# Optimization experiments

Hardware: AMD Instinct MI355X
Metric: run time of the kernel (lower is better)

## Reference

```python
import jax, jax.numpy as jnp
import numpy as np

NUM_TOURS = 200   # fixed segment count (original: tour_index.max()+1)
EPS = 1e-5        # torch InstanceNorm1d default eps


def setup_inputs() -> dict:
    key = jax.random.key(0)
    ks = jax.random.split(key, 9)
    B, P, D = 64, 2000, 128
    embeddings = jax.random.normal(ks[0], (B, P + 1, D), jnp.float32)
    tour_index = jax.random.randint(ks[1], (B, P), 0, NUM_TOURS, dtype=jnp.int32)
    # tour_combiner: Linear(2D -> D); feedforward: Linear(D -> D); stored as (in, out)
    W1 = jax.random.normal(ks[2], (2 * D, D), jnp.float32) / np.sqrt(2 * D)
    b1 = jax.random.normal(ks[3], (D,), jnp.float32) * 0.01
    W2 = jax.random.normal(ks[4], (D, D), jnp.float32) / np.sqrt(D)
    b2 = jax.random.normal(ks[5], (D,), jnp.float32) * 0.01
    # InstanceNorm1d affine params (per channel)
    gamma = 1.0 + 0.1 * jax.random.normal(ks[6], (D,), jnp.float32)
    beta = 0.1 * jax.random.normal(ks[7], (D,), jnp.float32)
    return {
        "batch_size": B, "num_customers": P,
        "tour_index": tour_index, "embeddings": embeddings,
        "W1": W1, "b1": b1, "W2": W2, "b2": b2,
        "gamma": gamma, "beta": beta,
    }


def reference(batch_size, num_customers, tour_index, embeddings, W1, b1, W2, b2, gamma, beta):
    B, P = batch_size, num_customers
    D = embeddings.shape[-1]
    cust = embeddings[:, 1:]                                  # (B, P, D)
    # tour-level segment sum (scatter_add over tour ids, per batch)
    flat_idx = (tour_index + jnp.arange(B, dtype=tour_index.dtype)[:, None] * NUM_TOURS).reshape(-1)
    tour_emb = jax.ops.segment_sum(cust.reshape(B * P, D), flat_idx,
                                   num_segments=B * NUM_TOURS).reshape(B, NUM_TOURS, D)
    # gather tour embedding back to each customer
    cust_tour = jnp.take_along_axis(tour_emb, tour_index[:, :, None], axis=1)  # (B, P, D)
    # concat -> linear -> relu -> linear
    combined = jnp.concatenate([cust, cust_tour], axis=-1)    # (B, P, 2D)
    h = jax.nn.relu(combined @ W1 + b1)
    h = h @ W2 + b2
    # residual + instance norm over the customer axis, per channel
    added = cust + h
    mean = jnp.mean(added, axis=1, keepdims=True)
    var = jnp.var(added, axis=1, keepdims=True)
    normed = (added - mean) * jax.lax.rsqrt(var + EPS) * gamma + beta
    return jnp.concatenate([embeddings[:, :1], normed], axis=1)
```

## Files before the change

kernel.cpp:

```cpp
#include <hip/hip_runtime.h>
#include <stdint.h>

typedef unsigned short u16;
typedef __attribute__((ext_vector_type(8))) short short8;
typedef __attribute__((ext_vector_type(4))) float floatx4;

constexpr int B_ = 64, P_ = 2000, D_ = 128, T_ = 200;

__device__ __forceinline__ u16 f2bf(float f) {
  union { float f; uint32_t u; } v; v.f = f;
  return (u16)((v.u + 0x7fffu + ((v.u >> 16) & 1u)) >> 16);
}

__global__ __launch_bounds__(256) void k_pre(
    const int* __restrict__ tidx, int* __restrict__ list,
    int* __restrict__ goff, int* __restrict__ gcnt,
    const float* __restrict__ W1, const float* __restrict__ W2,
    u16* __restrict__ w1f, u16* __restrict__ w2f, float* __restrict__ ssum) {
  __shared__ int tix[P_];
  __shared__ int cnt[256], scan[256], cur[256];
  const int bid = blockIdx.x, tid = threadIdx.x;

  if (bid >= 64) {
    if (bid < 128) {
      ssum[(bid - 64) * 256 + tid] = 0.f;
      return;
    }
    int t = (bid - 128) * 256 + tid;
    if (t >= 6144) return;
    const float* W = (t < 4096) ? W1 : W2;
    u16* dst = (t < 4096) ? w1f : w2f;
    int fid = (t < 4096) ? t : t - 4096;
    int lane = fid & 63;
    int nt = (fid >> 6) & 7;
    int ks = fid >> 9;
    int quad = lane >> 4, c = lane & 15;
    int k0 = ks * 32 + quad * 8;
#pragma unroll
    for (int j = 0; j < 8; ++j)
      dst[(size_t)fid * 8 + j] = f2bf(W[(k0 + j) * D_ + nt * 16 + c]);
    return;
  }

  const int b = bid;
  cnt[tid] = 0;
  for (int i = tid; i < P_; i += 256) tix[i] = tidx[b * P_ + i];
  __syncthreads();
  for (int i = tid; i < P_; i += 256) atomicAdd(&cnt[tix[i]], 1);
  __syncthreads();
  scan[tid] = cnt[tid];
  __syncthreads();
  for (int s = 1; s < 256; s <<= 1) {
    int v = (tid >= s) ? scan[tid - s] : 0;
    __syncthreads();
    scan[tid] += v;
    __syncthreads();
  }
  int excl = scan[tid] - cnt[tid];
  if (tid < T_) {
    goff[b * T_ + tid] = excl;
    gcnt[b * T_ + tid] = cnt[tid];
  }
  cur[tid] = excl;
  __syncthreads();
  for (int i = tid; i < P_; i += 256) {
    int slot = atomicAdd(&cur[tix[i]], 1);
    list[b * P_ + slot] = i;
  }
}

__global__ __launch_bounds__(256) void k_gather(const float* __restrict__ emb,
                                                const int* __restrict__ list,
                                                const int* __restrict__ goff,
                                                const int* __restrict__ gcnt,
                                                u16* __restrict__ tourb) {
  const int tid = threadIdx.x;
  const int lane = tid & 63, wv = tid >> 6;
  const int seg = blockIdx.x * 4 + wv;
  const int b = seg / T_;
  const int off = goff[seg], cn = gcnt[seg];
  const int* lstb = list + b * P_;
  const float* eb = emb + ((size_t)(b * 2001 + 1)) * D_ + lane * 2;
  float sx = 0.f, sy = 0.f;
  for (int i = 0; i < cn; i += 8) {
    int pr[8];
#pragma unroll
    for (int j = 0; j < 8; ++j)
      if (i + j < cn) pr[j] = lstb[off + i + j];
    float2 v[8];
#pragma unroll
    for (int j = 0; j < 8; ++j)
      if (i + j < cn) v[j] = *(const float2*)(eb + (size_t)pr[j] * D_);
#pragma unroll
    for (int j = 0; j < 8; ++j)
      if (i + j < cn) { sx += v[j].x; sy += v[j].y; }
  }
  uint32_t pk = (uint32_t)f2bf(sx) | ((uint32_t)f2bf(sy) << 16);
  ((uint32_t*)(tourb + (size_t)seg * D_))[lane] = pk;
}

__global__ __launch_bounds__(256, 8) void k_mlp(
    const int* __restrict__ tidx, const float* __restrict__ emb,
    const u16* __restrict__ tourb,
    const u16* __restrict__ w1f, const u16* __restrict__ w2f,
    const float* __restrict__ b1, const float* __restrict__ b2,
    float* __restrict__ ssum, float* __restrict__ ssq,
    float* __restrict__ out) {
  __shared__ u16 hbuf[64 * 136];
  __shared__ float red[2][2][128];
  const int tid = threadIdx.x;
  const int w = tid >> 6, lane = tid & 63, quad = lane >> 4, c = lane & 15;
  const int base = blockIdx.x * 64;
  const int r0 = w * 16;

  for (int i = tid; i < 512; i += 256) ((float*)red)[i] = 0.f;

  const int blo = base / P_;
  const int bhi = (base + 63) / P_;
  const bool straddle = (blo != bhi);
  const int bsplit = bhi * P_;

  const int m0 = base + r0 + c;
  const int ab = m0 / P_, ap = m0 - ab * P_;
  const float* arow = emb + ((size_t)(ab * 2001 + 1 + ap)) * D_;
  const u16* trow = tourb + ((size_t)(ab * T_ + tidx[m0])) * D_;

  float bias1[8], bias2[8];
#pragma unroll
  for (int nt = 0; nt < 8; ++nt) {
    bias1[nt] = b1[nt * 16 + c];
    bias2[nt] = b2[nt * 16 + c];
  }

  floatx4 acc[8];
#pragma unroll
  for (int nt = 0; nt < 8; ++nt) acc[nt] = (floatx4)0.f;

#pragma unroll
  for (int ks = 0; ks < 8; ++ks) {
    short8 a;
    if (ks < 4) {
      const float* src = arow + ks * 32 + quad * 8;
      floatx4 x0 = *(const floatx4*)src;
      floatx4 x1 = *(const floatx4*)(src + 4);
#pragma unroll
      for (int j = 0; j < 4; ++j) {
        a[j]     = (short)f2bf(x0[j]);
        a[4 + j] = (short)f2bf(x1[j]);
      }
    } else {
      a = *(const short8*)(trow + (ks - 4) * 32 + quad * 8);
    }
#pragma unroll
    for (int nt = 0; nt < 8; ++nt) {
      short8 bf = *(const short8*)(w1f + ((size_t)((ks * 8 + nt) * 64 + lane)) * 8);
      acc[nt] = __builtin_amdgcn_mfma_f32_16x16x32_bf16(a, bf, acc[nt], 0, 0, 0);
    }
  }

#pragma unroll
  for (int nt = 0; nt < 8; ++nt)
#pragma unroll
    for (int r = 0; r < 4; ++r) {
      int row = r0 + quad * 4 + r;
      float v = acc[nt][r] + bias1[nt];
      hbuf[row * 136 + nt * 16 + c] = f2bf(v > 0.f ? v : 0.f);
    }
  __syncthreads();

  floatx4 acc2[8];
#pragma unroll
  for (int nt = 0; nt < 8; ++nt) acc2[nt] = (floatx4)0.f;

#pragma unroll
  for (int ks = 0; ks < 4; ++ks) {
    short8 a = *(const short8*)(&hbuf[(r0 + c) * 136 + ks * 32 + quad * 8]);
#pragma unroll
    for (int nt = 0; nt < 8; ++nt) {
      short8 bf = *(const short8*)(w2f + ((size_t)((ks * 8 + nt) * 64 + lane)) * 8);
      acc2[nt] = __builtin_amdgcn_mfma_f32_16x16x32_bf16(a, bf, acc2[nt], 0, 0, 0);
    }
  }

  float s[8], q[8];
#pragma unroll
  for (int nt = 0; nt < 8; ++nt) { s[nt] = 0.f; q[nt] = 0.f; }
#pragma unroll
  for (int nt = 0; nt < 8; ++nt)
#pragma unroll
    for (int r = 0; r < 4; ++r) {
      int row = r0 + quad * 4 + r;
      int m = base + row;
      int b = m / P_, p = m - b * P_;
      size_t gaddr = ((size_t)(b * 2001 + 1 + p)) * D_ + nt * 16 + c;
      float v = emb[gaddr] + (acc2[nt][r] + bias2[nt]);
      out[gaddr] = v;
      if (!straddle || m < bsplit) {
        s[nt] += v; q[nt] += v * v;
      } else {
        atomicAdd(&red[1][0][nt * 16 + c], v);
        atomicAdd(&red[1][1][nt * 16 + c], v * v);
      }
    }
#pragma unroll
  for (int nt = 0; nt < 8; ++nt) {
    s[nt] += __shfl_xor(s[nt], 16);
    s[nt] += __shfl_xor(s[nt], 32);
    q[nt] += __shfl_xor(q[nt], 16);
    q[nt] += __shfl_xor(q[nt], 32);
  }
  if (quad == 0) {
#pragma unroll
    for (int nt = 0; nt < 8; ++nt) {
      atomicAdd(&red[0][0][nt * 16 + c], s[nt]);
      atomicAdd(&red[0][1][nt * 16 + c], q[nt]);
    }
  }
  __syncthreads();
  if (tid < 128) {
    atomicAdd(&ssum[blo * D_ + tid], red[0][0][tid]);
    if (straddle) atomicAdd(&ssum[bhi * D_ + tid], red[1][0][tid]);
  } else {
    int col = tid - 128;
    atomicAdd(&ssq[blo * D_ + col], red[0][1][col]);
    if (straddle) atomicAdd(&ssq[bhi * D_ + col], red[1][1][col]);
  }
}

__global__ __launch_bounds__(256) void k_out(
    const float* __restrict__ emb,
    const float* __restrict__ ssum, const float* __restrict__ ssq,
    const float* __restrict__ gamma, const float* __restrict__ beta,
    float* __restrict__ out) {
  size_t i = ((size_t)blockIdx.x * 256 + threadIdx.x) * 8;
  int row = (int)(i >> 7), col = (int)(i & 127);
  int b = row / 2001, r = row - b * 2001;
  if (r == 0) {
    *(floatx4*)(out + i)     = *(const floatx4*)(emb + i);
    *(floatx4*)(out + i + 4) = *(const floatx4*)(emb + i + 4);
  } else {
    floatx4 a0 = *(const floatx4*)(out + i);
    floatx4 a1 = *(const floatx4*)(out + i + 4);
    int cc = b * D_ + col;
    floatx4 su0 = *(const floatx4*)(ssum + cc);
    floatx4 su1 = *(const floatx4*)(ssum + cc + 4);
    floatx4 sq0 = *(const floatx4*)(ssq + cc);
    floatx4 sq1 = *(const floatx4*)(ssq + cc + 4);
    floatx4 g0  = *(const floatx4*)(gamma + col);
    floatx4 g1  = *(const floatx4*)(gamma + col + 4);
    floatx4 be0 = *(const floatx4*)(beta + col);
    floatx4 be1 = *(const floatx4*)(beta + col + 4);
    constexpr float invP = 1.f / P_;
#pragma unroll
    for (int j = 0; j < 4; ++j) {
      float mean = su0[j] * invP;
      float var  = sq0[j] * invP - mean * mean;
      float sc   = rsqrtf(var + 1e-5f) * g0[j];
      a0[j] = a0[j] * sc + (be0[j] - mean * sc);
      float mean1 = su1[j] * invP;
      float var1  = sq1[j] * invP - mean1 * mean1;
      float sc1   = rsqrtf(var1 + 1e-5f) * g1[j];
      a1[j] = a1[j] * sc1 + (be1[j] - mean1 * sc1);
    }
    *(floatx4*)(out + i)     = a0;
    *(floatx4*)(out + i + 4) = a1;
  }
}

extern "C" void kernel_launch(void* const* d_in, const int* in_sizes, int n_in,
                              void* d_out, int out_size, void* d_ws, size_t ws_size,
                              hipStream_t stream) {
  const int*   tour_index = (const int*)d_in[2];
  const float* emb   = (const float*)d_in[3];
  const float* W1    = (const float*)d_in[4];
  const float* b1    = (const float*)d_in[5];
  const float* W2    = (const float*)d_in[6];
  const float* b2    = (const float*)d_in[7];
  const float* gamma = (const float*)d_in[8];
  const float* beta  = (const float*)d_in[9];
  float* out = (float*)d_out;
  char* ws = (char*)d_ws;

  u16*   w1f   = (u16*)(ws);
  u16*   w2f   = (u16*)(ws + 65536);
  float* ssum  = (float*)(ws + 98304);
  float* ssq   = ssum + B_ * D_;
  u16*   tourb = (u16*)(ws + 229376);
  int*   list  = (int*)(ws + 3506176);
  int*   goff  = (int*)(ws + 4018176);
  int*   gcnt  = (int*)(ws + 4069376);

  hipLaunchKernelGGL(k_pre,    dim3(152),  dim3(256), 0, stream,
                     tour_index, list, goff, gcnt, W1, W2, w1f, w2f, ssum);
  hipLaunchKernelGGL(k_gather, dim3(3200), dim3(256), 0, stream, emb, list, goff, gcnt, tourb);
  hipLaunchKernelGGL(k_mlp,    dim3(2000), dim3(256), 0, stream, tour_index, emb, tourb,
                     w1f, w2f, b1, b2, ssum, ssq, out);
  hipLaunchKernelGGL(k_out,    dim3(8004), dim3(256), 0, stream, emb, ssum, ssq, gamma, beta, out);
}
```

Before: 247.4 us.

## Split MLP block work across waves by column halves, halving rows per block

Each k_mlp block now handles 32 rows instead of 64, with four waves arranged as 2 row-groups by 2 column-halves, so each wave computes only 4 of the 8 output column tiles. The grid doubles to 4000 blocks, and accumulator registers and shared memory per wave shrink. The aim is more parallelism and occupancy with lower register pressure. The cost is that each A row fragment is loaded and converted twice (once per column half), and there are twice as many blocks doing the global ssum/ssq atomics.

```diff
diff --git a/kernel.cpp b/kernel.cpp
--- a/kernel.cpp
+++ b/kernel.cpp
@@ -106,17 +106,18 @@
     const float* __restrict__ b1, const float* __restrict__ b2,
     float* __restrict__ ssum, float* __restrict__ ssq,
     float* __restrict__ out) {
-  __shared__ u16 hbuf[64 * 136];
+  __shared__ u16 hbuf[32 * 136];
   __shared__ float red[2][2][128];
   const int tid = threadIdx.x;
   const int w = tid >> 6, lane = tid & 63, quad = lane >> 4, c = lane & 15;
-  const int base = blockIdx.x * 64;
-  const int r0 = w * 16;
+  const int wr = w >> 1, wc = w & 1;
+  const int base = blockIdx.x * 32;
+  const int r0 = wr * 16;
 
   for (int i = tid; i < 512; i += 256) ((float*)red)[i] = 0.f;
 
   const int blo = base / P_;
-  const int bhi = (base + 63) / P_;
+  const int bhi = (base + 31) / P_;
   const bool straddle = (blo != bhi);
   const int bsplit = bhi * P_;
 
@@ -125,16 +126,16 @@
   const float* arow = emb + ((size_t)(ab * 2001 + 1 + ap)) * D_;
   const u16* trow = tourb + ((size_t)(ab * T_ + tidx[m0])) * D_;
 
-  float bias1[8], bias2[8];
-#pragma unroll
-  for (int nt = 0; nt < 8; ++nt) {
-    bias1[nt] = b1[nt * 16 + c];
-    bias2[nt] = b2[nt * 16 + c];
-  }
-
-  floatx4 acc[8];
-#pragma unroll
-  for (int nt = 0; nt < 8; ++nt) acc[nt] = (floatx4)0.f;
+  float bias1[4], bias2[4];
+#pragma unroll
+  for (int ntl = 0; ntl < 4; ++ntl) {
+    bias1[ntl] = b1[(wc * 4 + ntl) * 16 + c];
+    bias2[ntl] = b2[(wc * 4 + ntl) * 16 + c];
+  }
+
+  floatx4 acc[4];
+#pragma unroll
+  for (int ntl = 0; ntl < 4; ++ntl) acc[ntl] = (floatx4)0.f;
 
 #pragma unroll
   for (int ks = 0; ks < 8; ++ks) {
@@ -152,68 +153,72 @@
       a = *(const short8*)(trow + (ks - 4) * 32 + quad * 8);
     }
 #pragma unroll
-    for (int nt = 0; nt < 8; ++nt) {
+    for (int ntl = 0; ntl < 4; ++ntl) {
+      int nt = wc * 4 + ntl;
       short8 bf = *(const short8*)(w1f + ((size_t)((ks * 8 + nt) * 64 + lane)) * 8);
-      acc[nt] = __builtin_amdgcn_mfma_f32_16x16x32_bf16(a, bf, acc[nt], 0, 0, 0);
-    }
-  }
-
-#pragma unroll
-  for (int nt = 0; nt < 8; ++nt)
+      acc[ntl] = __builtin_amdgcn_mfma_f32_16x16x32_bf16(a, bf, acc[ntl], 0, 0, 0);
+    }
+  }
+
+#pragma unroll
+  for (int ntl = 0; ntl < 4; ++ntl)
 #pragma unroll
     for (int r = 0; r < 4; ++r) {
       int row = r0 + quad * 4 + r;
-      float v = acc[nt][r] + bias1[nt];
-      hbuf[row * 136 + nt * 16 + c] = f2bf(v > 0.f ? v : 0.f);
-    }
-  __syncthreads();
-
-  floatx4 acc2[8];
-#pragma unroll
-  for (int nt = 0; nt < 8; ++nt) acc2[nt] = (floatx4)0.f;
+      float v = acc[ntl][r] + bias1[ntl];
+      hbuf[row * 136 + wc * 64 + ntl * 16 + c] = f2bf(v > 0.f ? v : 0.f);
+    }
+  __syncthreads();
+
+  floatx4 acc2[4];
+#pragma unroll
+  for (int ntl = 0; ntl < 4; ++ntl) acc2[ntl] = (floatx4)0.f;
 
 #pragma unroll
   for (int ks = 0; ks < 4; ++ks) {
     short8 a = *(const short8*)(&hbuf[(r0 + c) * 136 + ks * 32 + quad * 8]);
 #pragma unroll
-    for (int nt = 0; nt < 8; ++nt) {
+    for (int ntl = 0; ntl < 4; ++ntl) {
+      int nt = wc * 4 + ntl;
       short8 bf = *(const short8*)(w2f + ((size_t)((ks * 8 + nt) * 64 + lane)) * 8);
-      acc2[nt] = __builtin_amdgcn_mfma_f32_16x16x32_bf16(a, bf, acc2[nt], 0, 0, 0);
-    }
-  }
-
-  float s[8], q[8];
-#pragma unroll
-  for (int nt = 0; nt < 8; ++nt) { s[nt] = 0.f; q[nt] = 0.f; }
-#pragma unroll
-  for (int nt = 0; nt < 8; ++nt)
+      acc2[ntl] = __builtin_amdgcn_mfma_f32_16x16x32_bf16(a, bf, acc2[ntl], 0, 0, 0);
+    }
+  }
+
+  float s[4], q[4];
+#pragma unroll
+  for (int ntl = 0; ntl < 4; ++ntl) { s[ntl] = 0.f; q[ntl] = 0.f; }
+#pragma unroll
+  for (int ntl = 0; ntl < 4; ++ntl)
 #pragma unroll
     for (int r = 0; r < 4; ++r) {
       int row = r0 + quad * 4 + r;
       int m = base + row;
       int b = m / P_, p = m - b * P_;
-      size_t gaddr = ((size_t)(b * 2001 + 1 + p)) * D_ + nt * 16 + c;
-      float v = emb[gaddr] + (acc2[nt][r] + bias2[nt]);
+      int col = wc * 64 + ntl * 16 + c;
+      size_t gaddr = ((size_t)(b * 2001 + 1 + p)) * D_ + col;
+      float v = emb[gaddr] + (acc2[ntl][r] + bias2[ntl]);
       out[gaddr] = v;
       if (!straddle || m < bsplit) {
-        s[nt] += v; q[nt] += v * v;
+        s[ntl] += v; q[ntl] += v * v;
       } else {
-        atomicAdd(&red[1][0][nt * 16 + c], v);
-        atomicAdd(&red[1][1][nt * 16 + c], v * v);
+        atomicAdd(&red[1][0][col], v);
+        atomicAdd(&red[1][1][col], v * v);
       }
     }
 #pragma unroll
-  for (int nt = 0; nt < 8; ++nt) {
-    s[nt] += __shfl_xor(s[nt], 16);
-    s[nt] += __shfl_xor(s[nt], 32);
-    q[nt] += __shfl_xor(q[nt], 16);
-    q[nt] += __shfl_xor(q[nt], 32);
+  for (int ntl = 0; ntl < 4; ++ntl) {
+    s[ntl] += __shfl_xor(s[ntl], 16);
+    s[ntl] += __shfl_xor(s[ntl], 32);
+    q[ntl] += __shfl_xor(q[ntl], 16);
+    q[ntl] += __shfl_xor(q[ntl], 32);
   }
   if (quad == 0) {
 #pragma unroll
-    for (int nt = 0; nt < 8; ++nt) {
-      atomicAdd(&red[0][0][nt * 16 + c], s[nt]);
-      atomicAdd(&red[0][1][nt * 16 + c], q[nt]);
+    for (int ntl = 0; ntl < 4; ++ntl) {
+      int col = wc * 64 + ntl * 16 + c;
+      atomicAdd(&red[0][0][col], s[ntl]);
+      atomicAdd(&red[0][1][col], q[ntl]);
     }
   }
   __syncthreads();
@@ -293,7 +298,7 @@
   hipLaunchKernelGGL(k_pre,    dim3(152),  dim3(256), 0, stream,
                      tour_index, list, goff, gcnt, W1, W2, w1f, w2f, ssum);
   hipLaunchKernelGGL(k_gather, dim3(3200), dim3(256), 0, stream, emb, list, goff, gcnt, tourb);
-  hipLaunchKernelGGL(k_mlp,    dim3(2000), dim3(256), 0, stream, tour_index, emb, tourb,
+  hipLaunchKernelGGL(k_mlp,    dim3(4000), dim3(256), 0, stream, tour_index, emb, tourb,
                      w1f, w2f, b1, b2, ssum, ssq, out);
   hipLaunchKernelGGL(k_out,    dim3(8004), dim3(256), 0, stream, emb, ssum, ssq, gamma, beta, out);
 }
```

New measurement: 222.3 us. 1.11x faster.
